# Optimization experiments

Hardware: AMD Instinct MI355X
Metric: run time of the kernel (lower is better)

## Reference

```python
import jax, jax.numpy as jnp
import numpy as np

N, E = 50000, 800000          # nodes, edges (self-loops added in reference)
IN_C, HID, OUT_C = 512, 128, 40
K, H = 4, 8                   # n_layers, heads
C = HID // H                  # per-head channels = 16
L = K + 1                     # with_initial_residual=True -> K+1 convs
NEG_SLOPE = 0.2               # PyG GATConv default leaky_relu slope


def setup_inputs():
    key = jax.random.key(0)
    ks = jax.random.split(key, 12)
    s = 0.05
    x = jax.random.normal(ks[0], (N, IN_C), jnp.float32)
    edge_index = jax.random.randint(ks[1], (2, E), 0, N, dtype=jnp.int32)
    fc0_w = jax.random.normal(ks[2], (IN_C, HID), jnp.float32) * s
    fc0_b = jax.random.normal(ks[3], (HID,), jnp.float32) * s
    lin_w = jax.random.normal(ks[4], (L, HID, HID), jnp.float32) * s      # GATConv lin (bias=False)
    att_src = jax.random.normal(ks[5], (L, H, C), jnp.float32) * s
    att_dst = jax.random.normal(ks[6], (L, H, C), jnp.float32) * s
    conv_bias = jax.random.normal(ks[7], (L, HID), jnp.float32) * s
    alphas = jnp.zeros((L,), jnp.float32).at[0].set(1.0)                  # init_alphas: t[0]=1
    fc1_w = jax.random.normal(ks[8], (HID, OUT_C), jnp.float32) * s
    fc1_b = jax.random.normal(ks[9], (OUT_C,), jnp.float32) * s
    return {"x": x, "edge_index": edge_index, "fc0_w": fc0_w, "fc0_b": fc0_b,
            "lin_w": lin_w, "att_src": att_src, "att_dst": att_dst,
            "conv_bias": conv_bias, "alphas": alphas, "fc1_w": fc1_w, "fc1_b": fc1_b}


def _gat_conv(h, src, dst, lin_w, a_src_w, a_dst_w, bias):
    # PyG GATConv (eval mode): linear -> edgewise attention -> segment softmax -> scatter-sum
    hp = (h @ lin_w).reshape(N, H, C)                 # [N,H,C]
    a_src = jnp.einsum('nhc,hc->nh', hp, a_src_w)     # [N,H]
    a_dst = jnp.einsum('nhc,hc->nh', hp, a_dst_w)
    e = jax.nn.leaky_relu(a_src[src] + a_dst[dst], NEG_SLOPE)   # [E+N,H]
    emax = jax.ops.segment_max(e, dst, num_segments=N)          # per-dst, per-head max
    e = jnp.exp(e - emax[dst])
    denom = jax.ops.segment_sum(e, dst, num_segments=N)
    alpha = e / (denom[dst] + 1e-16)                            # segment softmax
    msg = hp[src] * alpha[:, :, None]                           # [E+N,H,C]
    out = jax.ops.segment_sum(msg, dst, num_segments=N)         # [N,H,C]
    return out.reshape(N, H * C) + bias


def reference(x, edge_index, fc0_w, fc0_b, lin_w, att_src, att_dst, conv_bias, alphas, fc1_w, fc1_b):
    # forward_clenshawRes, eval mode (dropout = identity, batchNorm=False)
    loops = jnp.arange(N, dtype=edge_index.dtype)
    src = jnp.concatenate([edge_index[0], loops])   # add self-loops (PyG default)
    dst = jnp.concatenate([edge_index[1], loops])
    h0 = x @ fc0_w + fc0_b                          # fcs[0]
    last = jnp.zeros_like(h0)
    second_last = jnp.zeros_like(h0)
    for i in range(L):
        hcur = jax.nn.elu(_gat_conv(last, src, dst, lin_w[i], att_src[i], att_dst[i], conv_bias[i]))
        hcur = 2.0 * hcur - second_last + alphas[L - 1 - i] * h0   # alphas[-(i+1)]
        second_last, last = last, hcur
    out = last @ fc1_w + fc1_b                      # fcs[-1]
    return jax.nn.log_softmax(out, axis=1)
```

## Files before the change

### kernel.cpp

```cpp
#include <hip/hip_runtime.h>
#include <math.h>

#define NN      50000
#define E_CNT   800000
#define IN_C    512
#define HID     128
#define OUT_C   40
#define NHEAD   8
#define CPH     16
#define NLAYER  5
#define NEG     0.2f
#define CAP     64
#define NCOL    144

typedef __attribute__((ext_vector_type(8))) short bf16x8;
typedef __attribute__((ext_vector_type(4))) float f32x4;

__device__ __forceinline__ float lrelu(float x) { return x > 0.f ? x : NEG * x; }
__device__ __forceinline__ float eluf(float x)  { return x > 0.f ? x : expm1f(x); }

__device__ __forceinline__ float bf2f(unsigned short u) {
    union { unsigned int a; float f; } v; v.a = ((unsigned int)u) << 16;
    return v.f;
}
__device__ __forceinline__ float2 bf2f2(unsigned int u) {
    union { unsigned int a; float f; } lo, hi;
    lo.a = u << 16; hi.a = u & 0xffff0000u;
    return make_float2(lo.f, hi.f);
}
__device__ __forceinline__ unsigned short f2bf(float f) {
    union { float f; unsigned int u; } v; v.f = f;
    return (unsigned short)((v.u + 0x7fffu + ((v.u >> 16) & 1u)) >> 16);
}
__device__ __forceinline__ unsigned int pack2(float a, float b) {
    return ((unsigned int)f2bf(b) << 16) | f2bf(a);
}

__device__ __forceinline__ void gl2lds16(const void* g, void* l) {
    __builtin_amdgcn_global_load_lds(
        (const __attribute__((address_space(1))) unsigned int*)g,
        (__attribute__((address_space(3))) unsigned int*)l, 16, 0, 0);
}

__global__ __launch_bounds__(256) void k_wt(const float* __restrict__ w,
                                            unsigned short* __restrict__ wt, int K, int opitch) {
    __shared__ float t[32][33];
    const float* ws = w + (size_t)blockIdx.z * K * HID;
    unsigned short* wd = wt + (size_t)blockIdx.z * opitch;
    int k0 = blockIdx.x * 32, n0 = blockIdx.y * 32;
    int tx = threadIdx.x & 31, ty = threadIdx.x >> 5;
    for (int r = ty; r < 32; r += 8) t[r][tx] = ws[(size_t)(k0 + r) * HID + n0 + tx];
    __syncthreads();
    for (int r = ty; r < 32; r += 8) wd[(size_t)(n0 + r) * K + k0 + tx] = f2bf(t[tx][r]);
}

__global__ void k_watt(const float* __restrict__ linw, const float* __restrict__ attS,
                       const float* __restrict__ attD, unsigned short* __restrict__ wt2) {
    int i = blockIdx.x * blockDim.x + threadIdx.x;
    if (i >= 4 * 16 * HID) return;
    int l = i >> 11, r = (i >> 7) & 15, k = i & 127;
    int h = r & 7, isD = r >> 3;
    const float* W = linw + (size_t)(l + 1) * HID * HID;
    const float* av = (isD ? attD : attS) + (size_t)(l + 1) * NHEAD * CPH + h * CPH;
    float s = 0.f;
#pragma unroll
    for (int c = 0; c < CPH; ++c) s += W[(size_t)k * HID + h * CPH + c] * av[c];
    wt2[(size_t)l * NCOL * HID + (size_t)(128 + r) * HID + k] = f2bf(s);
}

__global__ void k_wout(const float* __restrict__ w, unsigned short* __restrict__ wt1) {
    int i = blockIdx.x * blockDim.x + threadIdx.x;
    if (i >= 48 * HID) return;
    int r = i >> 7, k = i & 127;
    wt1[i] = (r < OUT_C) ? f2bf(w[(size_t)k * OUT_C + r]) : (unsigned short)0;
}

template<int K, int A_F32, int NT, int EPI>
__global__ __launch_bounds__(256) void k_mgemm(const void* __restrict__ aptr,
                                               const unsigned short* __restrict__ wt,
                                               const float* __restrict__ bias,
                                               const float* __restrict__ cb0,
                                               const float* __restrict__ alphas,
                                               unsigned short* __restrict__ out_b,
                                               unsigned short* __restrict__ out_h0,
                                               float* __restrict__ aSo,
                                               float* __restrict__ aDo) {
    __shared__ unsigned short As[64 * 32];
    __shared__ unsigned short Bs[NT * 16 * 32];
    const int tid  = threadIdx.x;
    const int w    = tid >> 6, lane = tid & 63;
    const int fr   = lane & 15, fq = lane >> 4;
    const int row0 = blockIdx.x * 64;
    const int rowb = row0 + w * 16;
    const int rs = lane >> 2;
    const int ko = (lane & 3) * 8;
    f32x4 acc[NT] = {};

    for (int k0 = 0; k0 < K; k0 += 32) {
        if (A_F32) {
            int row = tid >> 2, kb = (tid & 3) * 8;
            int grow = row0 + row; if (grow >= NN) grow = NN - 1;
            const float* s = (const float*)aptr + (size_t)grow * K + k0 + kb;
            float4 v0 = *(const float4*)s, v1 = *(const float4*)(s + 4);
            union { bf16x8 v; unsigned int u[4]; } pk;
            pk.u[0] = pack2(v0.x, v0.y); pk.u[1] = pack2(v0.z, v0.w);
            pk.u[2] = pack2(v1.x, v1.y); pk.u[3] = pack2(v1.z, v1.w);
            *(bf16x8*)&As[row * 32 + kb] = pk.v;
            for (int j = w; j < NT; j += 4)
                gl2lds16(wt + (size_t)(j * 16 + rs) * K + k0 + ko, &Bs[j * 16 * 32]);
        } else {
            for (int c = w; c < 4 + NT; c += 4) {
                if (c < 4) {
                    int grow = row0 + c * 16 + rs; if (grow >= NN) grow = NN - 1;
                    gl2lds16((const unsigned short*)aptr + (size_t)grow * K + k0 + ko,
                             &As[c * 16 * 32]);
                } else {
                    int j = c - 4;
                    gl2lds16(wt + (size_t)(j * 16 + rs) * K + k0 + ko, &Bs[j * 16 * 32]);
                }
            }
        }
        __syncthreads();
        bf16x8 af = *(const bf16x8*)&As[(w * 16 + fr) * 32 + fq * 8];
#pragma unroll
        for (int t = 0; t < NT; ++t) {
            bf16x8 bfr = *(const bf16x8*)&Bs[(t * 16 + fr) * 32 + fq * 8];
            acc[t] = __builtin_amdgcn_mfma_f32_16x16x32_bf16(af, bfr, acc[t], 0, 0, 0);
        }
        __syncthreads();
    }

    const int cl = lane & 15, rq = (lane >> 4) * 4;
    const float a4 = (EPI == 2) ? alphas[NLAYER - 1] : 0.f;
#pragma unroll
    for (int t = 0; t < 8; ++t) {
        int col = t * 16 + cl;
        float bcol = (EPI == 2) ? bias[col] : 0.f;
        float ecol = (EPI == 2) ? 2.f * eluf(cb0[col]) : 0.f;
#pragma unroll
        for (int rg = 0; rg < 4; ++rg) {
            int row = rowb + rq + rg;
            if (row < NN) {
                if (EPI == 0) {
                    out_b[(size_t)row * HID + col] = f2bf(acc[t][rg]);
                } else {
                    float h0v = acc[t][rg] + bcol;
                    out_h0[(size_t)row * HID + col] = f2bf(h0v);
                    out_b[(size_t)row * HID + col]  = f2bf(ecol + a4 * h0v);
                }
            }
        }
    }
    if (NT == 9) {
#pragma unroll
        for (int rg = 0; rg < 4; ++rg) {
            int row = rowb + rq + rg;
            if (row < NN) {
                float v = acc[8][rg];
                if (cl < 8) aSo[(size_t)row * NHEAD + cl] = v;
                else        aDo[(size_t)row * NHEAD + (cl - 8)] = v;
            }
        }
    }
}

__global__ __launch_bounds__(256) void k_out(const unsigned short* __restrict__ ab,
                                             const unsigned short* __restrict__ wt1,
                                             const float* __restrict__ b,
                                             float* __restrict__ out) {
    __shared__ unsigned short As[64 * 32];
    __shared__ unsigned short Bs[48 * 32];
    const int tid  = threadIdx.x;
    const int w    = tid >> 6, lane = tid & 63;
    const int fr   = lane & 15, fq = lane >> 4;
    const int row0 = blockIdx.x * 64;
    const int rowb = row0 + w * 16;
    const int rs = lane >> 2;
    const int ko = (lane & 3) * 8;
    f32x4 acc[3] = {};

    for (int k0 = 0; k0 < HID; k0 += 32) {
        for (int c = w; c < 7; c += 4) {
            if (c < 4) {
                int grow = row0 + c * 16 + rs; if (grow >= NN) grow = NN - 1;
                gl2lds16(ab + (size_t)grow * HID + k0 + ko, &As[c * 16 * 32]);
            } else {
                int j = c - 4;
                gl2lds16(wt1 + (size_t)(j * 16 + rs) * HID + k0 + ko, &Bs[j * 16 * 32]);
            }
        }
        __syncthreads();
        bf16x8 af = *(const bf16x8*)&As[(w * 16 + fr) * 32 + fq * 8];
#pragma unroll
        for (int t = 0; t < 3; ++t) {
            bf16x8 bfr = *(const bf16x8*)&Bs[(t * 16 + fr) * 32 + fq * 8];
            acc[t] = __builtin_amdgcn_mfma_f32_16x16x32_bf16(af, bfr, acc[t], 0, 0, 0);
        }
        __syncthreads();
    }

    const int cl = lane & 15, rq = (lane >> 4) * 4;
    float b3[3];
#pragma unroll
    for (int t = 0; t < 3; ++t) {
        int col = t * 16 + cl;
        b3[t] = (col < OUT_C) ? b[col] : 0.f;
    }
#pragma unroll
    for (int rg = 0; rg < 4; ++rg) {
        int row = rowb + rq + rg;
        float v[3];
        float mx = -1e30f;
#pragma unroll
        for (int t = 0; t < 3; ++t) {
            int col = t * 16 + cl;
            v[t] = acc[t][rg] + b3[t];
            if (col < OUT_C) mx = fmaxf(mx, v[t]);
        }
#pragma unroll
        for (int off = 1; off < 16; off <<= 1) mx = fmaxf(mx, __shfl_xor(mx, off));
        float sum = 0.f;
#pragma unroll
        for (int t = 0; t < 3; ++t) {
            int col = t * 16 + cl;
            if (col < OUT_C) sum += __expf(v[t] - mx);
        }
#pragma unroll
        for (int off = 1; off < 16; off <<= 1) sum += __shfl_xor(sum, off);
        float lse = mx + logf(sum);
        if (row < NN) {
#pragma unroll
            for (int t = 0; t < 3; ++t) {
                int col = t * 16 + cl;
                if (col < OUT_C) out[(size_t)row * OUT_C + col] = v[t] - lse;
            }
        }
    }
}

__global__ void k_hist(const int* __restrict__ dst, int* __restrict__ deg) {
    int e = blockIdx.x * blockDim.x + threadIdx.x;
    if (e < E_CNT) atomicAdd(&deg[dst[e]], 1);
}

__global__ __launch_bounds__(1024) void k_part(const int* __restrict__ deg, int* __restrict__ part) {
    int i = blockIdx.x * 1024 + threadIdx.x;
    int v = (i < NN) ? deg[i] : 0;
    for (int off = 32; off; off >>= 1) v += __shfl_down(v, off);
    __shared__ int ws[16];
    if ((threadIdx.x & 63) == 0) ws[threadIdx.x >> 6] = v;
    __syncthreads();
    if (threadIdx.x < 16) {
        int t = ws[threadIdx.x];
        for (int off = 8; off; off >>= 1) t += __shfl_down(t, off);
        if (threadIdx.x == 0) part[blockIdx.x] = t;
    }
}

__global__ void k_scanpart(int* __restrict__ part, int* __restrict__ rowstart, int nb) {
    int t = threadIdx.x;
    int v = (t < nb) ? part[t] : 0;
    int x = v;
    for (int off = 1; off < 64; off <<= 1) { int u = __shfl_up(x, off); if (t >= off) x += u; }
    if (t < nb) part[t] = x - v;
    if (t == nb - 1) rowstart[NN] = x;
}

__global__ __launch_bounds__(1024) void k_scanblk(const int* __restrict__ deg,
                                                  const int* __restrict__ partx,
                                                  int* __restrict__ rowstart,
                                                  int* __restrict__ cursor) {
    int b = blockIdx.x, t = threadIdx.x, i = b * 1024 + t;
    int v = (i < NN) ? deg[i] : 0;
    int x = v;
    for (int off = 1; off < 64; off <<= 1) { int u = __shfl_up(x, off); if ((t & 63) >= off) x += u; }
    __shared__ int ws[16];
    if ((t & 63) == 63) ws[t >> 6] = x;
    __syncthreads();
    if (t < 64) {
        int wv = (t < 16) ? ws[t] : 0;
        for (int off = 1; off < 16; off <<= 1) { int u = __shfl_up(wv, off); if (t >= off) wv += u; }
        if (t < 16) ws[t] = wv;
    }
    __syncthreads();
    int waveoff = (t >= 64) ? ws[(t >> 6) - 1] : 0;
    int excl = x - v + waveoff + partx[b];
    if (i < NN) { rowstart[i] = excl; cursor[i] = excl; }
}

__global__ void k_scatter(const int* __restrict__ src, const int* __restrict__ dst,
                          int* __restrict__ cursor, int* __restrict__ csr) {
    int e = blockIdx.x * blockDim.x + threadIdx.x;
    if (e < E_CNT) {
        int p = atomicAdd(&cursor[dst[e]], 1);
        csr[p] = src[e];
    }
}

__global__ __launch_bounds__(256) void k_agg(
    const unsigned short* __restrict__ hpb, const float* __restrict__ aS, const float* __restrict__ aD,
    const int* __restrict__ rowstart, const int* __restrict__ csr,
    const float* __restrict__ bias, const unsigned short* __restrict__ h0b,
    const unsigned short* __restrict__ slb, const float* __restrict__ alphas, int aidx, int sl_zero,
    unsigned int* __restrict__ outb) {
    __shared__ int   slds[4][CAP];
    __shared__ float wlds[4][CAP][NHEAD];
    const int wave = threadIdx.x >> 6;
    const int lane = threadIdx.x & 63;
    const int n    = blockIdx.x * 4 + wave;
    const int rsb  = rowstart[n];
    const int deg  = rowstart[n + 1] - rsb;
    const int cnt  = deg < CAP ? deg : CAP;

    for (int j = lane; j < cnt; j += 64) slds[wave][j] = csr[rsb + j];
    __syncthreads();

    const int h    = lane & 7;
    const int slot = lane >> 3;
    const float adst = aD[n * NHEAD + h];

    float den = 0.f;
#pragma unroll
    for (int t = 0; t < 8; ++t) {
        int j = slot + t * 8;
        if (j < cnt) {
            int s = slds[wave][j];
            float wv = __expf(lrelu(aS[s * NHEAD + h] + adst));
            wlds[wave][j][h] = wv;
            den += wv;
        }
    }
    for (int j = CAP + slot; j < deg; j += 8)
        den += __expf(lrelu(aS[csr[rsb + j] * NHEAD + h] + adst));
#pragma unroll
    for (int off = 8; off < 64; off <<= 1) den += __shfl_xor(den, off);
    const float w0 = __expf(lrelu(aS[n * NHEAD + h] + adst));
    den += w0;
    const float dinv = 1.f / (den + 1e-16f);
    __syncthreads();

    const int l  = lane & 15;
    const int q  = lane >> 4;
    const int hh = l >> 1;
    const float w0h = __shfl(w0, hh);
    const float dih = __shfl(dinv, hh);
    const float adh = __shfl(adst, hh);

    float c0 = 0.f, c1 = 0.f, c2 = 0.f, c3 = 0.f, c4 = 0.f, c5 = 0.f, c6 = 0.f, c7 = 0.f;
    if (q == 0) {
        uint4 u = *(const uint4*)(hpb + (size_t)n * HID + 8 * l);
        float2 p0 = bf2f2(u.x), p1 = bf2f2(u.y), p2 = bf2f2(u.z), p3 = bf2f2(u.w);
        c0 = w0h * p0.x; c1 = w0h * p0.y; c2 = w0h * p1.x; c3 = w0h * p1.y;
        c4 = w0h * p2.x; c5 = w0h * p2.y; c6 = w0h * p3.x; c7 = w0h * p3.y;
    }
    if (deg <= CAP) {
#pragma unroll 2
        for (int j = q; j < deg; j += 4) {
            int s = slds[wave][j];
            float wv = wlds[wave][j][hh];
            uint4 u = *(const uint4*)(hpb + (size_t)s * HID + 8 * l);
            float2 p0 = bf2f2(u.x), p1 = bf2f2(u.y), p2 = bf2f2(u.z), p3 = bf2f2(u.w);
            c0 += wv * p0.x; c1 += wv * p0.y; c2 += wv * p1.x; c3 += wv * p1.y;
            c4 += wv * p2.x; c5 += wv * p2.y; c6 += wv * p3.x; c7 += wv * p3.y;
        }
    } else {
        for (int j = q; j < deg; j += 4) {
            int s; float wv;
            if (j < CAP) { s = slds[wave][j]; wv = wlds[wave][j][hh]; }
            else { s = csr[rsb + j]; wv = __expf(lrelu(aS[s * NHEAD + hh] + adh)); }
            uint4 u = *(const uint4*)(hpb + (size_t)s * HID + 8 * l);
            float2 p0 = bf2f2(u.x), p1 = bf2f2(u.y), p2 = bf2f2(u.z), p3 = bf2f2(u.w);
            c0 += wv * p0.x; c1 += wv * p0.y; c2 += wv * p1.x; c3 += wv * p1.y;
            c4 += wv * p2.x; c5 += wv * p2.y; c6 += wv * p3.x; c7 += wv * p3.y;
        }
    }
    c0 += __shfl_xor(c0, 16); c1 += __shfl_xor(c1, 16); c2 += __shfl_xor(c2, 16); c3 += __shfl_xor(c3, 16);
    c4 += __shfl_xor(c4, 16); c5 += __shfl_xor(c5, 16); c6 += __shfl_xor(c6, 16); c7 += __shfl_xor(c7, 16);
    c0 += __shfl_xor(c0, 32); c1 += __shfl_xor(c1, 32); c2 += __shfl_xor(c2, 32); c3 += __shfl_xor(c3, 32);
    c4 += __shfl_xor(c4, 32); c5 += __shfl_xor(c5, 32); c6 += __shfl_xor(c6, 32); c7 += __shfl_xor(c7, 32);

    if (q == 0) {
        float4 bv0 = ((const float4*)bias)[2 * l];
        float4 bv1 = ((const float4*)bias)[2 * l + 1];
        float g0 = eluf(c0 * dih + bv0.x);
        float g1 = eluf(c1 * dih + bv0.y);
        float g2 = eluf(c2 * dih + bv0.z);
        float g3 = eluf(c3 * dih + bv0.w);
        float g4 = eluf(c4 * dih + bv1.x);
        float g5 = eluf(c5 * dih + bv1.y);
        float g6 = eluf(c6 * dih + bv1.z);
        float g7 = eluf(c7 * dih + bv1.w);
        const float ac = alphas[aidx];
        float s0 = 0.f, s1 = 0.f, s2 = 0.f, s3 = 0.f, s4 = 0.f, s5 = 0.f, s6 = 0.f, s7 = 0.f;
        if (!sl_zero) {
            uint4 su = *(const uint4*)(slb + (size_t)n * HID + 8 * l);
            float2 p0 = bf2f2(su.x), p1 = bf2f2(su.y), p2 = bf2f2(su.z), p3 = bf2f2(su.w);
            s0 = p0.x; s1 = p0.y; s2 = p1.x; s3 = p1.y; s4 = p2.x; s5 = p2.y; s6 = p3.x; s7 = p3.y;
        }
        float hx0 = 0.f, hx1 = 0.f, hx2 = 0.f, hx3 = 0.f, hx4 = 0.f, hx5 = 0.f, hx6 = 0.f, hx7 = 0.f;
        if (ac != 0.f) {
            uint4 hu = *(const uint4*)(h0b + (size_t)n * HID + 8 * l);
            float2 p0 = bf2f2(hu.x), p1 = bf2f2(hu.y), p2 = bf2f2(hu.z), p3 = bf2f2(hu.w);
            hx0 = p0.x; hx1 = p0.y; hx2 = p1.x; hx3 = p1.y; hx4 = p2.x; hx5 = p2.y; hx6 = p3.x; hx7 = p3.y;
        }
        uint4 pb;
        pb.x = pack2(2.f * g0 - s0 + ac * hx0, 2.f * g1 - s1 + ac * hx1);
        pb.y = pack2(2.f * g2 - s2 + ac * hx2, 2.f * g3 - s3 + ac * hx3);
        pb.z = pack2(2.f * g4 - s4 + ac * hx4, 2.f * g5 - s5 + ac * hx5);
        pb.w = pack2(2.f * g6 - s6 + ac * hx6, 2.f * g7 - s7 + ac * hx7);
        ((uint4*)outb)[(size_t)n * 16 + l] = pb;
    }
}

extern "C" void kernel_launch(void* const* d_in, const int* in_sizes, int n_in,
                              void* d_out, int out_size, void* d_ws, size_t ws_size,
                              hipStream_t stream) {
    const float* x      = (const float*)d_in[0];
    const int*   ei     = (const int*)  d_in[1];
    const float* fc0w   = (const float*)d_in[2];
    const float* fc0b   = (const float*)d_in[3];
    const float* linw   = (const float*)d_in[4];
    const float* attS   = (const float*)d_in[5];
    const float* attD   = (const float*)d_in[6];
    const float* cbias  = (const float*)d_in[7];
    const float* alphas = (const float*)d_in[8];
    const float* fc1w   = (const float*)d_in[9];
    const float* fc1b   = (const float*)d_in[10];
    float* out = (float*)d_out;

    char* p = (char*)d_ws;
    auto alloc = [&](size_t bytes) { void* q = (void*)p; p += (bytes + 255) / 256 * 256; return q; };
    const size_t NB16 = (size_t)NN * HID * 2;
    unsigned short* h0b  = (unsigned short*)alloc(NB16);
    unsigned short* Lb0  = (unsigned short*)alloc(NB16);
    unsigned short* Lb1  = (unsigned short*)alloc(NB16);
    unsigned short* Lb2  = (unsigned short*)alloc(NB16);
    unsigned short* hpb  = (unsigned short*)alloc(NB16);
    float* aSb = (float*)alloc((size_t)NN * NHEAD * 4);
    float* aDb = (float*)alloc((size_t)NN * NHEAD * 4);
    unsigned short* WT0 = (unsigned short*)alloc((size_t)HID * IN_C * 2);
    unsigned short* WT2 = (unsigned short*)alloc((size_t)4 * NCOL * HID * 2);
    unsigned short* WT1 = (unsigned short*)alloc((size_t)48 * HID * 2);
    int* deg      = (int*)alloc((size_t)(NN + 1) * 4);
    int* rowstart = (int*)alloc((size_t)(NN + 1) * 4);
    int* part     = (int*)alloc(64 * 4);
    int* csr      = (int*)alloc((size_t)E_CNT * 4);
    int* cursor   = deg;

    const int* esrc = ei;
    const int* edst = ei + E_CNT;
    const int NB = (NN + 1023) / 1024;

    hipMemsetAsync(deg, 0, (size_t)NN * 4, stream);
    k_hist<<<(E_CNT + 255) / 256, 256, 0, stream>>>(edst, deg);
    k_part<<<NB, 1024, 0, stream>>>(deg, part);
    k_scanpart<<<1, 64, 0, stream>>>(part, rowstart, NB);
    k_scanblk<<<NB, 1024, 0, stream>>>(deg, part, rowstart, cursor);
    k_scatter<<<(E_CNT + 255) / 256, 256, 0, stream>>>(esrc, edst, cursor, csr);

    {
        dim3 g0(IN_C / 32, HID / 32, 1);
        k_wt<<<g0, 256, 0, stream>>>(fc0w, WT0, IN_C, HID * IN_C);
        dim3 gl(HID / 32, HID / 32, 4);
        k_wt<<<gl, 256, 0, stream>>>(linw + (size_t)HID * HID, WT2, HID, NCOL * HID);
        k_watt<<<(4 * 16 * HID + 255) / 256, 256, 0, stream>>>(linw, attS, attD, WT2);
        k_wout<<<(48 * HID + 255) / 256, 256, 0, stream>>>(fc1w, WT1);
    }

    const int GB = (NN + 63) / 64;
    k_mgemm<IN_C, 1, 8, 2><<<GB, 256, 0, stream>>>(x, WT0, fc0b, cbias, alphas,
                                                   Lb0, h0b, nullptr, nullptr);

    unsigned short* last = Lb0; unsigned short* sl = Lb1; unsigned short* nxt = Lb2;
    for (int i = 1; i < NLAYER; ++i) {
        k_mgemm<HID, 0, 9, 0><<<GB, 256, 0, stream>>>(last, WT2 + (size_t)(i - 1) * NCOL * HID,
                                                      nullptr, nullptr, nullptr, hpb, nullptr, aSb, aDb);
        k_agg<<<NN / 4, 256, 0, stream>>>(hpb, aSb, aDb, rowstart, csr,
                                          cbias + i * HID, h0b, sl, alphas, NLAYER - 1 - i, (i == 1) ? 1 : 0,
                                          (unsigned int*)nxt);
        unsigned short* tmp = sl; sl = last; last = nxt; nxt = tmp;
    }

    k_out<<<GB, 256, 0, stream>>>(last, WT1, fc1b, out);
}
```

Baseline: 544.2 us.

## Widen GEMM K-tile to 64, merge weight prep kernels, unroll aggregation gathers

The MFMA GEMM kernels now stage 64-wide K slices in LDS and issue two MFMA k-steps per barrier pair. This halves the number of sync and load rounds, at the cost of more shared memory per block. The four weight-preparation launches are merged into one flat elementwise kernel, which drops launch overhead but gives up the coalesced transpose. The aggregation loop for low-degree nodes is manually unrolled four ways so several independent row gathers are in flight at once.

```diff
diff --git a/kernel.cpp b/kernel.cpp
--- a/kernel.cpp
+++ b/kernel.cpp
@@ -19,10 +19,6 @@
 __device__ __forceinline__ float lrelu(float x) { return x > 0.f ? x : NEG * x; }
 __device__ __forceinline__ float eluf(float x)  { return x > 0.f ? x : expm1f(x); }
 
-__device__ __forceinline__ float bf2f(unsigned short u) {
-    union { unsigned int a; float f; } v; v.a = ((unsigned int)u) << 16;
-    return v.f;
-}
 __device__ __forceinline__ float2 bf2f2(unsigned int u) {
     union { unsigned int a; float f; } lo, hi;
     lo.a = u << 16; hi.a = u & 0xffff0000u;
@@ -42,37 +38,40 @@
         (__attribute__((address_space(3))) unsigned int*)l, 16, 0, 0);
 }
 
-__global__ __launch_bounds__(256) void k_wt(const float* __restrict__ w,
-                                            unsigned short* __restrict__ wt, int K, int opitch) {
-    __shared__ float t[32][33];
-    const float* ws = w + (size_t)blockIdx.z * K * HID;
-    unsigned short* wd = wt + (size_t)blockIdx.z * opitch;
-    int k0 = blockIdx.x * 32, n0 = blockIdx.y * 32;
-    int tx = threadIdx.x & 31, ty = threadIdx.x >> 5;
-    for (int r = ty; r < 32; r += 8) t[r][tx] = ws[(size_t)(k0 + r) * HID + n0 + tx];
-    __syncthreads();
-    for (int r = ty; r < 32; r += 8) wd[(size_t)(n0 + r) * K + k0 + tx] = f2bf(t[tx][r]);
-}
-
-__global__ void k_watt(const float* __restrict__ linw, const float* __restrict__ attS,
-                       const float* __restrict__ attD, unsigned short* __restrict__ wt2) {
+__global__ void k_prep(const float* __restrict__ fc0w, const float* __restrict__ linw,
+                       const float* __restrict__ attS, const float* __restrict__ attD,
+                       const float* __restrict__ fc1w,
+                       unsigned short* __restrict__ WT0, unsigned short* __restrict__ WT2,
+                       unsigned short* __restrict__ WT1) {
     int i = blockIdx.x * blockDim.x + threadIdx.x;
-    if (i >= 4 * 16 * HID) return;
-    int l = i >> 11, r = (i >> 7) & 15, k = i & 127;
-    int h = r & 7, isD = r >> 3;
-    const float* W = linw + (size_t)(l + 1) * HID * HID;
-    const float* av = (isD ? attD : attS) + (size_t)(l + 1) * NHEAD * CPH + h * CPH;
-    float s = 0.f;
-#pragma unroll
-    for (int c = 0; c < CPH; ++c) s += W[(size_t)k * HID + h * CPH + c] * av[c];
-    wt2[(size_t)l * NCOL * HID + (size_t)(128 + r) * HID + k] = f2bf(s);
-}
-
-__global__ void k_wout(const float* __restrict__ w, unsigned short* __restrict__ wt1) {
-    int i = blockIdx.x * blockDim.x + threadIdx.x;
-    if (i >= 48 * HID) return;
-    int r = i >> 7, k = i & 127;
-    wt1[i] = (r < OUT_C) ? f2bf(w[(size_t)k * OUT_C + r]) : (unsigned short)0;
+    if (i < HID * IN_C) {
+        int r = i >> 9, k = i & 511;
+        WT0[i] = f2bf(fc0w[(size_t)k * HID + r]);
+        return;
+    }
+    i -= HID * IN_C;
+    if (i < 4 * NCOL * HID) {
+        int l = i / (NCOL * HID);
+        int rem = i - l * (NCOL * HID);
+        int r = rem >> 7, k = rem & 127;
+        const float* W = linw + (size_t)(l + 1) * HID * HID;
+        if (r < HID) {
+            WT2[i] = f2bf(W[(size_t)k * HID + r]);
+        } else {
+            int r2 = r - HID, h = r2 & 7, isD = r2 >> 3;
+            const float* av = (isD ? attD : attS) + (size_t)(l + 1) * NHEAD * CPH + h * CPH;
+            float s = 0.f;
+#pragma unroll
+            for (int c = 0; c < CPH; ++c) s += W[(size_t)k * HID + h * CPH + c] * av[c];
+            WT2[i] = f2bf(s);
+        }
+        return;
+    }
+    i -= 4 * NCOL * HID;
+    if (i < 48 * HID) {
+        int r = i >> 7, k = i & 127;
+        WT1[i] = (r < OUT_C) ? f2bf(fc1w[(size_t)k * OUT_C + r]) : (unsigned short)0;
+    }
 }
 
 template<int K, int A_F32, int NT, int EPI>
@@ -85,47 +84,54 @@
                                                unsigned short* __restrict__ out_h0,
                                                float* __restrict__ aSo,
                                                float* __restrict__ aDo) {
-    __shared__ unsigned short As[64 * 32];
-    __shared__ unsigned short Bs[NT * 16 * 32];
+    __shared__ unsigned short As[64 * 64];
+    __shared__ unsigned short Bs[NT * 16 * 64];
     const int tid  = threadIdx.x;
     const int w    = tid >> 6, lane = tid & 63;
     const int fr   = lane & 15, fq = lane >> 4;
     const int row0 = blockIdx.x * 64;
     const int rowb = row0 + w * 16;
-    const int rs = lane >> 2;
-    const int ko = (lane & 3) * 8;
+    const int rg8  = lane >> 3;
+    const int kc8  = (lane & 7) * 8;
     f32x4 acc[NT] = {};
 
-    for (int k0 = 0; k0 < K; k0 += 32) {
+    for (int k0 = 0; k0 < K; k0 += 64) {
         if (A_F32) {
-            int row = tid >> 2, kb = (tid & 3) * 8;
+            int row = tid >> 2, kb = (tid & 3) * 16;
             int grow = row0 + row; if (grow >= NN) grow = NN - 1;
             const float* s = (const float*)aptr + (size_t)grow * K + k0 + kb;
             float4 v0 = *(const float4*)s, v1 = *(const float4*)(s + 4);
-            union { bf16x8 v; unsigned int u[4]; } pk;
-            pk.u[0] = pack2(v0.x, v0.y); pk.u[1] = pack2(v0.z, v0.w);
-            pk.u[2] = pack2(v1.x, v1.y); pk.u[3] = pack2(v1.z, v1.w);
-            *(bf16x8*)&As[row * 32 + kb] = pk.v;
-            for (int j = w; j < NT; j += 4)
-                gl2lds16(wt + (size_t)(j * 16 + rs) * K + k0 + ko, &Bs[j * 16 * 32]);
+            float4 v2 = *(const float4*)(s + 8), v3 = *(const float4*)(s + 12);
+            union { bf16x8 v; unsigned int u[4]; } p0, p1;
+            p0.u[0] = pack2(v0.x, v0.y); p0.u[1] = pack2(v0.z, v0.w);
+            p0.u[2] = pack2(v1.x, v1.y); p0.u[3] = pack2(v1.z, v1.w);
+            p1.u[0] = pack2(v2.x, v2.y); p1.u[1] = pack2(v2.z, v2.w);
+            p1.u[2] = pack2(v3.x, v3.y); p1.u[3] = pack2(v3.z, v3.w);
+            *(bf16x8*)&As[row * 64 + kb] = p0.v;
+            *(bf16x8*)&As[row * 64 + kb + 8] = p1.v;
+            for (int g = w; g < NT * 2; g += 4)
+                gl2lds16(wt + (size_t)(g * 8 + rg8) * K + k0 + kc8, &Bs[g * 8 * 64]);
         } else {
-            for (int c = w; c < 4 + NT; c += 4) {
-                if (c < 4) {
-                    int grow = row0 + c * 16 + rs; if (grow >= NN) grow = NN - 1;
-                    gl2lds16((const unsigned short*)aptr + (size_t)grow * K + k0 + ko,
-                             &As[c * 16 * 32]);
+            for (int g = w; g < 8 + NT * 2; g += 4) {
+                if (g < 8) {
+                    int grow = row0 + g * 8 + rg8; if (grow >= NN) grow = NN - 1;
+                    gl2lds16((const unsigned short*)aptr + (size_t)grow * K + k0 + kc8,
+                             &As[g * 8 * 64]);
                 } else {
-                    int j = c - 4;
-                    gl2lds16(wt + (size_t)(j * 16 + rs) * K + k0 + ko, &Bs[j * 16 * 32]);
+                    int j = g - 8;
+                    gl2lds16(wt + (size_t)(j * 8 + rg8) * K + k0 + kc8, &Bs[j * 8 * 64]);
                 }
             }
         }
         __syncthreads();
-        bf16x8 af = *(const bf16x8*)&As[(w * 16 + fr) * 32 + fq * 8];
-#pragma unroll
-        for (int t = 0; t < NT; ++t) {
-            bf16x8 bfr = *(const bf16x8*)&Bs[(t * 16 + fr) * 32 + fq * 8];
-            acc[t] = __builtin_amdgcn_mfma_f32_16x16x32_bf16(af, bfr, acc[t], 0, 0, 0);
+#pragma unroll
+        for (int kk = 0; kk < 2; ++kk) {
+            bf16x8 af = *(const bf16x8*)&As[(w * 16 + fr) * 64 + kk * 32 + fq * 8];
+#pragma unroll
+            for (int t = 0; t < NT; ++t) {
+                bf16x8 bfr = *(const bf16x8*)&Bs[(t * 16 + fr) * 64 + kk * 32 + fq * 8];
+                acc[t] = __builtin_amdgcn_mfma_f32_16x16x32_bf16(af, bfr, acc[t], 0, 0, 0);
+            }
         }
         __syncthreads();
     }
@@ -168,33 +174,36 @@
                                              const unsigned short* __restrict__ wt1,
                                              const float* __restrict__ b,
                                              float* __restrict__ out) {
-    __shared__ unsigned short As[64 * 32];
-    __shared__ unsigned short Bs[48 * 32];
+    __shared__ unsigned short As[64 * 64];
+    __shared__ unsigned short Bs[48 * 64];
     const int tid  = threadIdx.x;
     const int w    = tid >> 6, lane = tid & 63;
     const int fr   = lane & 15, fq = lane >> 4;
     const int row0 = blockIdx.x * 64;
     const int rowb = row0 + w * 16;
-    const int rs = lane >> 2;
-    const int ko = (lane & 3) * 8;
+    const int rg8  = lane >> 3;
+    const int kc8  = (lane & 7) * 8;
     f32x4 acc[3] = {};
 
-    for (int k0 = 0; k0 < HID; k0 += 32) {
-        for (int c = w; c < 7; c += 4) {
-            if (c < 4) {
-                int grow = row0 + c * 16 + rs; if (grow >= NN) grow = NN - 1;
-                gl2lds16(ab + (size_t)grow * HID + k0 + ko, &As[c * 16 * 32]);
+    for (int k0 = 0; k0 < HID; k0 += 64) {
+        for (int g = w; g < 14; g += 4) {
+            if (g < 8) {
+                int grow = row0 + g * 8 + rg8; if (grow >= NN) grow = NN - 1;
+                gl2lds16(ab + (size_t)grow * HID + k0 + kc8, &As[g * 8 * 64]);
             } else {
-                int j = c - 4;
-                gl2lds16(wt1 + (size_t)(j * 16 + rs) * HID + k0 + ko, &Bs[j * 16 * 32]);
+                int j = g - 8;
+                gl2lds16(wt1 + (size_t)(j * 8 + rg8) * HID + k0 + kc8, &Bs[j * 8 * 64]);
             }
         }
         __syncthreads();
-        bf16x8 af = *(const bf16x8*)&As[(w * 16 + fr) * 32 + fq * 8];
-#pragma unroll
-        for (int t = 0; t < 3; ++t) {
-            bf16x8 bfr = *(const bf16x8*)&Bs[(t * 16 + fr) * 32 + fq * 8];
-            acc[t] = __builtin_amdgcn_mfma_f32_16x16x32_bf16(af, bfr, acc[t], 0, 0, 0);
+#pragma unroll
+        for (int kk = 0; kk < 2; ++kk) {
+            bf16x8 af = *(const bf16x8*)&As[(w * 16 + fr) * 64 + kk * 32 + fq * 8];
+#pragma unroll
+            for (int t = 0; t < 3; ++t) {
+                bf16x8 bfr = *(const bf16x8*)&Bs[(t * 16 + fr) * 64 + kk * 32 + fq * 8];
+                acc[t] = __builtin_amdgcn_mfma_f32_16x16x32_bf16(af, bfr, acc[t], 0, 0, 0);
+            }
         }
         __syncthreads();
     }
@@ -347,21 +356,33 @@
     const float adh = __shfl(adst, hh);
 
     float c0 = 0.f, c1 = 0.f, c2 = 0.f, c3 = 0.f, c4 = 0.f, c5 = 0.f, c6 = 0.f, c7 = 0.f;
+    auto acc8 = [&](uint4 u, float wv) {
+        float2 p0 = bf2f2(u.x), p1 = bf2f2(u.y), p2 = bf2f2(u.z), p3 = bf2f2(u.w);
+        c0 += wv * p0.x; c1 += wv * p0.y; c2 += wv * p1.x; c3 += wv * p1.y;
+        c4 += wv * p2.x; c5 += wv * p2.y; c6 += wv * p3.x; c7 += wv * p3.y;
+    };
     if (q == 0) {
         uint4 u = *(const uint4*)(hpb + (size_t)n * HID + 8 * l);
-        float2 p0 = bf2f2(u.x), p1 = bf2f2(u.y), p2 = bf2f2(u.z), p3 = bf2f2(u.w);
-        c0 = w0h * p0.x; c1 = w0h * p0.y; c2 = w0h * p1.x; c3 = w0h * p1.y;
-        c4 = w0h * p2.x; c5 = w0h * p2.y; c6 = w0h * p3.x; c7 = w0h * p3.y;
+        acc8(u, w0h);
     }
     if (deg <= CAP) {
-#pragma unroll 2
-        for (int j = q; j < deg; j += 4) {
+        int j = q;
+        for (; j + 12 < deg; j += 16) {
+            int s0 = slds[wave][j],      s1 = slds[wave][j + 4];
+            int s2 = slds[wave][j + 8],  s3 = slds[wave][j + 12];
+            float v0 = wlds[wave][j][hh],      v1 = wlds[wave][j + 4][hh];
+            float v2 = wlds[wave][j + 8][hh],  v3 = wlds[wave][j + 12][hh];
+            uint4 u0 = *(const uint4*)(hpb + (size_t)s0 * HID + 8 * l);
+            uint4 u1 = *(const uint4*)(hpb + (size_t)s1 * HID + 8 * l);
+            uint4 u2 = *(const uint4*)(hpb + (size_t)s2 * HID + 8 * l);
+            uint4 u3 = *(const uint4*)(hpb + (size_t)s3 * HID + 8 * l);
+            acc8(u0, v0); acc8(u1, v1); acc8(u2, v2); acc8(u3, v3);
+        }
+        for (; j < deg; j += 4) {
             int s = slds[wave][j];
             float wv = wlds[wave][j][hh];
             uint4 u = *(const uint4*)(hpb + (size_t)s * HID + 8 * l);
-            float2 p0 = bf2f2(u.x), p1 = bf2f2(u.y), p2 = bf2f2(u.z), p3 = bf2f2(u.w);
-            c0 += wv * p0.x; c1 += wv * p0.y; c2 += wv * p1.x; c3 += wv * p1.y;
-            c4 += wv * p2.x; c5 += wv * p2.y; c6 += wv * p3.x; c7 += wv * p3.y;
+            acc8(u, wv);
         }
     } else {
         for (int j = q; j < deg; j += 4) {
@@ -369,9 +390,7 @@
             if (j < CAP) { s = slds[wave][j]; wv = wlds[wave][j][hh]; }
             else { s = csr[rsb + j]; wv = __expf(lrelu(aS[s * NHEAD + hh] + adh)); }
             uint4 u = *(const uint4*)(hpb + (size_t)s * HID + 8 * l);
-            float2 p0 = bf2f2(u.x), p1 = bf2f2(u.y), p2 = bf2f2(u.z), p3 = bf2f2(u.w);
-            c0 += wv * p0.x; c1 += wv * p0.y; c2 += wv * p1.x; c3 += wv * p1.y;
-            c4 += wv * p2.x; c5 += wv * p2.y; c6 += wv * p3.x; c7 += wv * p3.y;
+            acc8(u, wv);
         }
     }
     c0 += __shfl_xor(c0, 16); c1 += __shfl_xor(c1, 16); c2 += __shfl_xor(c2, 16); c3 += __shfl_xor(c3, 16);
@@ -458,14 +477,8 @@
     k_scanblk<<<NB, 1024, 0, stream>>>(deg, part, rowstart, cursor);
     k_scatter<<<(E_CNT + 255) / 256, 256, 0, stream>>>(esrc, edst, cursor, csr);
 
-    {
-        dim3 g0(IN_C / 32, HID / 32, 1);
-        k_wt<<<g0, 256, 0, stream>>>(fc0w, WT0, IN_C, HID * IN_C);
-        dim3 gl(HID / 32, HID / 32, 4);
-        k_wt<<<gl, 256, 0, stream>>>(linw + (size_t)HID * HID, WT2, HID, NCOL * HID);
-        k_watt<<<(4 * 16 * HID + 255) / 256, 256, 0, stream>>>(linw, attS, attD, WT2);
-        k_wout<<<(48 * HID + 255) / 256, 256, 0, stream>>>(fc1w, WT1);
-    }
+    const int PREP_N = HID * IN_C + 4 * NCOL * HID + 48 * HID;
+    k_prep<<<(PREP_N + 255) / 256, 256, 0, stream>>>(fc0w, linw, attS, attD, fc1w, WT0, WT2, WT1);
 
     const int GB = (NN + 63) / 64;
     k_mgemm<IN_C, 1, 8, 2><<<GB, 256, 0, stream>>>(x, WT0, fc0b, cbias, alphas,
```

Result: slower. 563.9 us (+3.6%).
